# Optimization experiments

Hardware: AMD Instinct MI355X
Metric: run time of the kernel (lower is better)

The kernel has to match this reference:

```python
import jax, jax.numpy as jnp
import numpy as np

N = 50000
E = 800000
H = 2          # heads
C = 64         # out channels per head (embedding_size)
NEG_SLOPE = 0.2


def setup_inputs() -> dict:
    key = jax.random.key(0)
    ks = jax.random.split(key, 8)
    x = jax.random.normal(ks[0], (N, 1), dtype=jnp.float32)
    edge_index = jax.random.randint(ks[1], (2, E), 0, N, dtype=jnp.int64)
    edge_attr = jax.random.normal(ks[2], (E, 1), dtype=jnp.float32)
    # GATv2Conv params: lin_l, lin_r (with bias), lin_edge (no bias), att, out bias
    W_l = jax.random.normal(ks[3], (1, H * C), dtype=jnp.float32)
    b_l = jnp.zeros((H * C,), dtype=jnp.float32)
    W_r = jax.random.normal(ks[4], (1, H * C), dtype=jnp.float32)
    b_r = jnp.zeros((H * C,), dtype=jnp.float32)
    W_e = jax.random.normal(ks[5], (1, H * C), dtype=jnp.float32)
    att = jax.random.normal(ks[6], (H, C), dtype=jnp.float32)
    bias = jnp.zeros((H * C,), dtype=jnp.float32)
    return {"x": x, "edge_index": edge_index, "edge_attr": edge_attr,
            "W_l": W_l, "b_l": b_l, "W_r": W_r, "b_r": b_r,
            "W_e": W_e, "att": att, "bias": bias}


def reference(x, edge_index, edge_attr, W_l, b_l, W_r, b_r, W_e, att, bias):
    n = x.shape[0]
    src, dst = edge_index[0], edge_index[1]

    # add_self_loops=True with fill_value='mean': self-loop edge_attr at node i
    # is the mean of incoming edge_attr (0 if no incoming edges).
    attr_sum = jax.ops.segment_sum(edge_attr, dst, num_segments=n)      # [N,1]
    cnt = jax.ops.segment_sum(jnp.ones((src.shape[0], 1), edge_attr.dtype), dst, num_segments=n)
    loop_attr = attr_sum / jnp.maximum(cnt, 1.0)                         # [N,1]

    loop = jnp.arange(n, dtype=src.dtype)
    src_f = jnp.concatenate([src, loop])                                 # [E+N]
    dst_f = jnp.concatenate([dst, loop])
    attr_f = jnp.concatenate([edge_attr, loop_attr], axis=0)             # [E+N,1]

    x_l = (x @ W_l + b_l).reshape(n, H, C)    # source transform
    x_r = (x @ W_r + b_r).reshape(n, H, C)    # target transform
    e = (attr_f @ W_e).reshape(-1, H, C)      # edge feature embedding

    # GATv2 attention: leaky_relu(x_l[j] + x_r[i] + e) . att
    g = jax.nn.leaky_relu(x_l[src_f] + x_r[dst_f] + e, NEG_SLOPE)        # [E+N,H,C]
    logits = jnp.einsum('ehc,hc->eh', g, att)                            # [E+N,H]

    # segment softmax grouped by destination node
    mx = jax.ops.segment_max(logits, dst_f, num_segments=n)              # [N,H]
    a = jnp.exp(logits - mx[dst_f])
    den = jax.ops.segment_sum(a, dst_f, num_segments=n)                  # [N,H]
    alpha = a / den[dst_f]                                               # [E+N,H]

    # weighted scatter-add of source messages
    out = jax.ops.segment_sum(alpha[:, :, None] * x_l[src_f], dst_f, num_segments=n)  # [N,H,C]
    return out.reshape(n, H * C) + bias
```

## Files before the change

### kernel.cpp

```cpp
#include <hip/hip_runtime.h>

#define NEG 0.2f

typedef float f4v __attribute__((ext_vector_type(4)));

__device__ __forceinline__ float leaky(float v){ return fmaxf(v, NEG * v); }

__device__ __forceinline__ int xcc_id(){
    int x;
    asm volatile("s_getreg_b32 %0, hwreg(HW_REG_XCC_ID)" : "=s"(x));
    return x & 7;
}

__global__ void __launch_bounds__(256) k_edge(
        const int* __restrict__ src, const int* __restrict__ dst,
        const float* __restrict__ attr, const float* __restrict__ x,
        const float* __restrict__ Wl, const float* __restrict__ Wr,
        const float* __restrict__ We, const float* __restrict__ bl,
        const float* __restrict__ br, const float* __restrict__ att,
        int* __restrict__ head, int* __restrict__ nxt,
        float4* __restrict__ payload, int E, int N){
    const int sub = threadIdx.x & 15;
    const float4* Wl4 = (const float4*)Wl;
    const float4* Wr4 = (const float4*)Wr;
    const float4* We4 = (const float4*)We;
    const float4* bl4 = (const float4*)bl;
    const float4* br4 = (const float4*)br;
    const float4* at4 = (const float4*)att;
    const int q = sub * 2;
    float4 wl0 = Wl4[q], wl1 = Wl4[q+1];
    float4 wr0 = Wr4[q], wr1 = Wr4[q+1];
    float4 we0 = We4[q], we1 = We4[q+1];
    float4 b0  = bl4[q], b1  = bl4[q+1];
    float4 c0  = br4[q], c1  = br4[q+1];
    float4 a0  = at4[q], a1  = at4[q+1];
    b0.x += c0.x; b0.y += c0.y; b0.z += c0.z; b0.w += c0.w;
    b1.x += c1.x; b1.y += c1.y; b1.z += c1.z; b1.w += c1.w;

    const int xcc = xcc_id();
    const int gid     = (blockIdx.x * 256 + threadIdx.x) >> 4;
    const int ngroups = (gridDim.x * 256) >> 4;

    for (int e = gid; e < E; e += ngroups){
        int s = src[e], d = dst[e];
        int prev = 0;
        if (sub == 0){
            size_t hidx = (size_t)((xcc << 1) | (e & 1)) * N + d;
            prev = __hip_atomic_exchange(&head[hidx], e,
                                         __ATOMIC_RELAXED,
                                         __HIP_MEMORY_SCOPE_WORKGROUP);
        }
        float xs = x[s], xd = x[d], a = attr[e];
        float acc;
        {
            float v0 = fmaf(xs, wl0.x, fmaf(xd, wr0.x, fmaf(a, we0.x, b0.x)));
            float v1 = fmaf(xs, wl0.y, fmaf(xd, wr0.y, fmaf(a, we0.y, b0.y)));
            float v2 = fmaf(xs, wl0.z, fmaf(xd, wr0.z, fmaf(a, we0.z, b0.z)));
            float v3 = fmaf(xs, wl0.w, fmaf(xd, wr0.w, fmaf(a, we0.w, b0.w)));
            acc  = leaky(v0) * a0.x;
            acc  = fmaf(leaky(v1), a0.y, acc);
            acc  = fmaf(leaky(v2), a0.z, acc);
            acc  = fmaf(leaky(v3), a0.w, acc);
            v0 = fmaf(xs, wl1.x, fmaf(xd, wr1.x, fmaf(a, we1.x, b1.x)));
            v1 = fmaf(xs, wl1.y, fmaf(xd, wr1.y, fmaf(a, we1.y, b1.y)));
            v2 = fmaf(xs, wl1.z, fmaf(xd, wr1.z, fmaf(a, we1.z, b1.z)));
            v3 = fmaf(xs, wl1.w, fmaf(xd, wr1.w, fmaf(a, we1.w, b1.w)));
            acc  = fmaf(leaky(v0), a1.x, acc);
            acc  = fmaf(leaky(v1), a1.y, acc);
            acc  = fmaf(leaky(v2), a1.z, acc);
            acc  = fmaf(leaky(v3), a1.w, acc);
        }
        acc += __shfl_xor(acc, 1);
        acc += __shfl_xor(acc, 2);
        acc += __shfl_xor(acc, 4);
        float other = __shfl_xor(acc, 8);
        if (sub == 0){
            f4v pv = { xs, a, acc, other };
            __builtin_nontemporal_store(pv, (f4v*)&payload[e]);
            __builtin_nontemporal_store(prev, &nxt[e]);
        }
    }
}

__global__ void __launch_bounds__(256) k_walk(
        const float* __restrict__ x,
        const int* __restrict__ head, const int* __restrict__ nxt,
        const float4* __restrict__ payload,
        const float* __restrict__ Wl, const float* __restrict__ Wr,
        const float* __restrict__ We, const float* __restrict__ bl,
        const float* __restrict__ br, const float* __restrict__ att,
        const float* __restrict__ bias,
        float4* __restrict__ out, int N){
    int t = blockIdx.x * 256 + threadIdx.x;
    int i = t >> 4, ln = t & 15;
    if (i >= N) return;

    const float4* Wl4 = (const float4*)Wl;
    const float4* Wr4 = (const float4*)Wr;
    const float4* We4 = (const float4*)We;
    const float4* bl4 = (const float4*)bl;
    const float4* br4 = (const float4*)br;
    const float4* at4 = (const float4*)att;
    const int q = ln * 2;
    float4 wl0 = Wl4[q], wl1 = Wl4[q+1];
    float4 wr0 = Wr4[q], wr1 = Wr4[q+1];
    float4 we0 = We4[q], we1 = We4[q+1];
    float4 b0  = bl4[q], b1  = bl4[q+1];
    float4 c0  = br4[q], c1  = br4[q+1];
    float4 a0  = at4[q], a1  = at4[q+1];
    wl0.x += wr0.x; wl0.y += wr0.y; wl0.z += wr0.z; wl0.w += wr0.w;
    wl1.x += wr1.x; wl1.y += wr1.y; wl1.z += wr1.z; wl1.w += wr1.w;
    b0.x += c0.x; b0.y += c0.y; b0.z += c0.z; b0.w += c0.w;
    b1.x += c1.x; b1.y += c1.y; b1.z += c1.z; b1.w += c1.w;

    float m0 = -3.4e38f, d0 = 0.f, n0 = 0.f;
    float m1 = -3.4e38f, d1 = 0.f, n1 = 0.f;
    float asum = 0.f;
    int deg = 0;
    for (int e = head[(size_t)ln * N + i]; e >= 0; e = nxt[e]){
        float4 v = payload[e];
        ++deg;
        asum += v.y;
        float mn0 = fmaxf(m0, v.z);
        float s0 = __expf(m0 - mn0), p0 = __expf(v.z - mn0);
        d0 = fmaf(d0, s0, p0);
        n0 = fmaf(n0, s0, p0 * v.x);
        m0 = mn0;
        float mn1 = fmaxf(m1, v.w);
        float s1 = __expf(m1 - mn1), p1 = __expf(v.w - mn1);
        d1 = fmaf(d1, s1, p1);
        n1 = fmaf(n1, s1, p1 * v.x);
        m1 = mn1;
    }
    #pragma unroll
    for (int off = 1; off < 16; off <<= 1){
        float om0 = __shfl_xor(m0, off), od0 = __shfl_xor(d0, off), on0 = __shfl_xor(n0, off);
        float om1 = __shfl_xor(m1, off), od1 = __shfl_xor(d1, off), on1 = __shfl_xor(n1, off);
        asum += __shfl_xor(asum, off);
        deg  += __shfl_xor(deg, off);
        float mn = fmaxf(m0, om0);
        d0 = d0 * __expf(m0 - mn) + od0 * __expf(om0 - mn);
        n0 = n0 * __expf(m0 - mn) + on0 * __expf(om0 - mn);
        m0 = mn;
        mn = fmaxf(m1, om1);
        d1 = d1 * __expf(m1 - mn) + od1 * __expf(om1 - mn);
        n1 = n1 * __expf(m1 - mn) + on1 * __expf(om1 - mn);
        m1 = mn;
    }
    float xi = x[i];
    float la = asum / (float)max(deg, 1);
    float pl;
    {
        float v0 = fmaf(xi, wl0.x, fmaf(la, we0.x, b0.x));
        float v1 = fmaf(xi, wl0.y, fmaf(la, we0.y, b0.y));
        float v2 = fmaf(xi, wl0.z, fmaf(la, we0.z, b0.z));
        float v3 = fmaf(xi, wl0.w, fmaf(la, we0.w, b0.w));
        pl  = leaky(v0) * a0.x;
        pl  = fmaf(leaky(v1), a0.y, pl);
        pl  = fmaf(leaky(v2), a0.z, pl);
        pl  = fmaf(leaky(v3), a0.w, pl);
        v0 = fmaf(xi, wl1.x, fmaf(la, we1.x, b1.x));
        v1 = fmaf(xi, wl1.y, fmaf(la, we1.y, b1.y));
        v2 = fmaf(xi, wl1.z, fmaf(la, we1.z, b1.z));
        v3 = fmaf(xi, wl1.w, fmaf(la, we1.w, b1.w));
        pl  = fmaf(leaky(v0), a1.x, pl);
        pl  = fmaf(leaky(v1), a1.y, pl);
        pl  = fmaf(leaky(v2), a1.z, pl);
        pl  = fmaf(leaky(v3), a1.w, pl);
    }
    pl += __shfl_xor(pl, 1);
    pl += __shfl_xor(pl, 2);
    pl += __shfl_xor(pl, 4);
    float other = __shfl_xor(pl, 8);
    float l0 = (ln < 8) ? pl : other;
    float l1 = (ln < 8) ? other : pl;
    {
        float mn = fmaxf(m0, l0);
        float s = __expf(m0 - mn), p = __expf(l0 - mn);
        d0 = fmaf(d0, s, p);
        n0 = fmaf(n0, s, p * xi);
    }
    {
        float mn = fmaxf(m1, l1);
        float s = __expf(m1 - mn), p = __expf(l1 - mn);
        d1 = fmaf(d1, s, p);
        n1 = fmaf(n1, s, p * xi);
    }
    float sres0 = n0 / d0;
    float sres1 = n1 / d1;

    const float* bs = bias;
    float4 w0 = Wl4[ln],      w1 = Wl4[ln + 16];
    float4 g0 = bl4[ln],      g1 = bl4[ln + 16];
    float4 z0 = ((const float4*)bs)[ln], z1 = ((const float4*)bs)[ln + 16];
    float4* orow = out + (size_t)i * 32;
    orow[ln]      = make_float4(fmaf(sres0, w0.x, g0.x + z0.x),
                                fmaf(sres0, w0.y, g0.y + z0.y),
                                fmaf(sres0, w0.z, g0.z + z0.z),
                                fmaf(sres0, w0.w, g0.w + z0.w));
    orow[ln + 16] = make_float4(fmaf(sres1, w1.x, g1.x + z1.x),
                                fmaf(sres1, w1.y, g1.y + z1.y),
                                fmaf(sres1, w1.z, g1.z + z1.z),
                                fmaf(sres1, w1.w, g1.w + z1.w));
}

extern "C" void kernel_launch(void* const* d_in, const int* in_sizes, int n_in,
                              void* d_out, int out_size, void* d_ws, size_t ws_size,
                              hipStream_t stream) {
    const float* x    = (const float*)d_in[0];
    const int*   ei   = (const int*)  d_in[1];
    const float* attr = (const float*)d_in[2];
    const float* Wl   = (const float*)d_in[3];
    const float* bl   = (const float*)d_in[4];
    const float* Wr   = (const float*)d_in[5];
    const float* br   = (const float*)d_in[6];
    const float* We   = (const float*)d_in[7];
    const float* att  = (const float*)d_in[8];
    const float* bias = (const float*)d_in[9];
    float* out = (float*)d_out;

    const int N = in_sizes[0];
    const int E = in_sizes[2];
    const int* src = ei;
    const int* dst = ei + E;

    char* w = (char*)d_ws;
    float4* payload = (float4*)w;
    int*    nxt     = (int*)(w + (size_t)E * 16);
    int*    head    = nxt + E;

    hipMemsetAsync(head, 0xFF, (size_t)16 * N * sizeof(int), stream);

    k_edge<<<2048, 256, 0, stream>>>(src, dst, attr, x,
                                     Wl, Wr, We, bl, br, att,
                                     head, nxt, payload, E, N);
    k_walk<<<(16 * N + 255) / 256, 256, 0, stream>>>(x, head, nxt, payload,
                                                     Wl, Wr, We, bl, br, att, bias,
                                                     (float4*)out, N);
}
```

Measured before the change: 79.51 us.

## Batch 16 edges per lane group with coalesced loads and node-interleaved head lists

k_edge now has each 16-lane group load 16 consecutive edges in a coalesced way, one per lane. It broadcasts each edge's inputs with shuffles so the group computes all 16 attention logits, then each lane writes its own payload. The per-XCC/parity head lists are replaced by 16 lists per node, laid out node-major (head[d*16+ln]), with device-scope atomicExch. The lists are selected by lane, which spreads atomic contention and makes the walk's head reads contiguous. The change also switches to a one-shot grid sized to E and adds an occupancy hint of 6 to launch_bounds. In exchange, lanes go idle during the serial loop over j and atomic scope widens.

```diff
diff --git a/kernel.cpp b/kernel.cpp
--- a/kernel.cpp
+++ b/kernel.cpp
@@ -6,28 +6,22 @@
 
 __device__ __forceinline__ float leaky(float v){ return fmaxf(v, NEG * v); }
 
-__device__ __forceinline__ int xcc_id(){
-    int x;
-    asm volatile("s_getreg_b32 %0, hwreg(HW_REG_XCC_ID)" : "=s"(x));
-    return x & 7;
-}
-
-__global__ void __launch_bounds__(256) k_edge(
+__global__ void __launch_bounds__(256, 6) k_edge(
         const int* __restrict__ src, const int* __restrict__ dst,
         const float* __restrict__ attr, const float* __restrict__ x,
         const float* __restrict__ Wl, const float* __restrict__ Wr,
         const float* __restrict__ We, const float* __restrict__ bl,
         const float* __restrict__ br, const float* __restrict__ att,
         int* __restrict__ head, int* __restrict__ nxt,
-        float4* __restrict__ payload, int E, int N){
-    const int sub = threadIdx.x & 15;
+        float4* __restrict__ payload, int E){
+    const int ln = threadIdx.x & 15;
     const float4* Wl4 = (const float4*)Wl;
     const float4* Wr4 = (const float4*)Wr;
     const float4* We4 = (const float4*)We;
     const float4* bl4 = (const float4*)bl;
     const float4* br4 = (const float4*)br;
     const float4* at4 = (const float4*)att;
-    const int q = sub * 2;
+    const int q = ln * 2;
     float4 wl0 = Wl4[q], wl1 = Wl4[q+1];
     float4 wr0 = Wr4[q], wr1 = Wr4[q+1];
     float4 we0 = We4[q], we1 = We4[q+1];
@@ -37,20 +31,27 @@
     b0.x += c0.x; b0.y += c0.y; b0.z += c0.z; b0.w += c0.w;
     b1.x += c1.x; b1.y += c1.y; b1.z += c1.z; b1.w += c1.w;
 
-    const int xcc = xcc_id();
-    const int gid     = (blockIdx.x * 256 + threadIdx.x) >> 4;
-    const int ngroups = (gridDim.x * 256) >> 4;
-
-    for (int e = gid; e < E; e += ngroups){
-        int s = src[e], d = dst[e];
-        int prev = 0;
-        if (sub == 0){
-            size_t hidx = (size_t)((xcc << 1) | (e & 1)) * N + d;
-            prev = __hip_atomic_exchange(&head[hidx], e,
-                                         __ATOMIC_RELAXED,
-                                         __HIP_MEMORY_SCOPE_WORKGROUP);
-        }
-        float xs = x[s], xd = x[d], a = attr[e];
+    const int gid  = (blockIdx.x * 256 + threadIdx.x) >> 4;
+    const int base = gid * 16;
+    if (base >= E) return;
+
+    const int eL = base + ln;
+    const bool val = eL < E;
+    int   sL = 0, dL = 0;
+    float aL = 0.f;
+    if (val){ sL = src[eL]; dL = dst[eL]; aL = attr[eL]; }
+    float xsL = val ? x[sL] : 0.f;
+    float xdL = val ? x[dL] : 0.f;
+    int prevL = 0;
+    if (val)
+        prevL = atomicExch(&head[dL * 16 + ln], eL);
+
+    const int cnt = min(16, E - base);
+    float l0L = 0.f, l1L = 0.f;
+    for (int j = 0; j < cnt; ++j){
+        float xs = __shfl(xsL, j, 16);
+        float xd = __shfl(xdL, j, 16);
+        float a  = __shfl(aL,  j, 16);
         float acc;
         {
             float v0 = fmaf(xs, wl0.x, fmaf(xd, wr0.x, fmaf(a, we0.x, b0.x)));
@@ -74,15 +75,19 @@
         acc += __shfl_xor(acc, 2);
         acc += __shfl_xor(acc, 4);
         float other = __shfl_xor(acc, 8);
-        if (sub == 0){
-            f4v pv = { xs, a, acc, other };
-            __builtin_nontemporal_store(pv, (f4v*)&payload[e]);
-            __builtin_nontemporal_store(prev, &nxt[e]);
+        if (ln == j){
+            l0L = (j < 8) ? acc : other;
+            l1L = (j < 8) ? other : acc;
         }
     }
+    if (val){
+        f4v pv = { xsL, aL, l0L, l1L };
+        __builtin_nontemporal_store(pv, (f4v*)&payload[eL]);
+        __builtin_nontemporal_store(prevL, &nxt[eL]);
+    }
 }
 
-__global__ void __launch_bounds__(256) k_walk(
+__global__ void __launch_bounds__(256, 6) k_walk(
         const float* __restrict__ x,
         const int* __restrict__ head, const int* __restrict__ nxt,
         const float4* __restrict__ payload,
@@ -117,7 +122,7 @@
     float m1 = -3.4e38f, d1 = 0.f, n1 = 0.f;
     float asum = 0.f;
     int deg = 0;
-    for (int e = head[(size_t)ln * N + i]; e >= 0; e = nxt[e]){
+    for (int e = head[(size_t)i * 16 + ln]; e >= 0; e = nxt[e]){
         float4 v = payload[e];
         ++deg;
         asum += v.y;
@@ -189,10 +194,9 @@
     float sres0 = n0 / d0;
     float sres1 = n1 / d1;
 
-    const float* bs = bias;
     float4 w0 = Wl4[ln],      w1 = Wl4[ln + 16];
     float4 g0 = bl4[ln],      g1 = bl4[ln + 16];
-    float4 z0 = ((const float4*)bs)[ln], z1 = ((const float4*)bs)[ln + 16];
+    float4 z0 = ((const float4*)bias)[ln], z1 = ((const float4*)bias)[ln + 16];
     float4* orow = out + (size_t)i * 32;
     orow[ln]      = make_float4(fmaf(sres0, w0.x, g0.x + z0.x),
                                 fmaf(sres0, w0.y, g0.y + z0.y),
@@ -231,10 +235,12 @@
 
     hipMemsetAsync(head, 0xFF, (size_t)16 * N * sizeof(int), stream);
 
-    k_edge<<<2048, 256, 0, stream>>>(src, dst, attr, x,
-                                     Wl, Wr, We, bl, br, att,
-                                     head, nxt, payload, E, N);
-    k_walk<<<(16 * N + 255) / 256, 256, 0, stream>>>(x, head, nxt, payload,
-                                                     Wl, Wr, We, bl, br, att, bias,
-                                                     (float4*)out, N);
+    int egroups = (E + 15) / 16;
+    int eblocks = (egroups + 15) / 16;
+    k_edge<<<eblocks, 256, 0, stream>>>(src, dst, attr, x,
+                                        Wl, Wr, We, bl, br, att,
+                                        head, nxt, payload, E);
+    k_walk<<<((size_t)16 * N + 255) / 256, 256, 0, stream>>>(x, head, nxt, payload,
+                                                             Wl, Wr, We, bl, br, att, bias,
+                                                             (float4*)out, N);
 }
```

After: 79.43 us. Within noise of the previous version (-0.1%).
